# Performance work log

Measured on AMD Instinct MI355X. Metric: run time of the kernel, lower is better.

## Reference

```python
import jax, jax.numpy as jnp
import numpy as np

DIM = 256
HID = 128


def setup_inputs() -> dict:
    key = jax.random.key(0)
    ks = jax.random.split(key, 10)
    B, T = 8, 2048
    s_in = 1.0 / np.sqrt(DIM)
    s_h = 1.0 / np.sqrt(HID)
    return {
        "x": jax.random.normal(ks[0], (B, T, DIM), jnp.float32),
        "adapt_bias": jax.random.normal(ks[1], (B, T, T), jnp.float32),
        "Wq": jax.random.uniform(ks[2], (HID, DIM), jnp.float32, -s_in, s_in),
        "bq": jax.random.uniform(ks[3], (HID,), jnp.float32, -s_in, s_in),
        "Wk": jax.random.uniform(ks[4], (HID, DIM), jnp.float32, -s_in, s_in),
        "bk": jax.random.uniform(ks[5], (HID,), jnp.float32, -s_in, s_in),
        "Wv": jax.random.uniform(ks[6], (HID, DIM), jnp.float32, -s_in, s_in),
        "bv": jax.random.uniform(ks[7], (HID,), jnp.float32, -s_in, s_in),
        "Wp": jax.random.uniform(ks[8], (DIM, HID), jnp.float32, -s_h, s_h),
        "bp": jax.random.uniform(ks[9], (DIM,), jnp.float32, -s_h, s_h),
    }


def reference(x, adapt_bias, Wq, bq, Wk, bk, Wv, bv, Wp, bp):
    # y = x (default). Q,K,V: [B,T,H]
    Q = jnp.einsum('btd,hd->bth', x, Wq) + bq
    K = jnp.einsum('btd,hd->bth', x, Wk) + bk
    V = jnp.einsum('btd,hd->bth', x, Wv) + bv
    Q_sig = jax.nn.sigmoid(Q)
    ab = jax.nn.softmax(adapt_bias, axis=-1)        # [B,T,T]
    Ksm = jax.nn.softmax(K, axis=1)                 # softmax over time dim
    eab = jnp.exp(ab)                               # [B,T,T]
    eK = jnp.exp(Ksm)                               # [B,T,H]
    num = jnp.einsum('bts,bsh->bth', eab, eK * V)
    den = jnp.einsum('bts,bsh->bth', eab, eK)
    Yt = Q_sig * (num / den)                        # [B,T,H]
    return jnp.einsum('bth,dh->btd', Yt, Wp) + bp   # [B,T,DIM]
```

## Files before the change

### kernel.cpp

```cpp
#include <hip/hip_runtime.h>
#include <hip/hip_bf16.h>

#define B_ 8
#define T_ 2048
#define D_ 256
#define H_ 128

typedef float f32x4 __attribute__((ext_vector_type(4)));
typedef short bf16x8 __attribute__((ext_vector_type(8)));

__device__ __forceinline__ unsigned short f2bf(float f){
  union { float f; unsigned u; } v; v.f = f;
  unsigned u = v.u;
  unsigned r = (u + 0x7FFFu + ((u >> 16) & 1u)) >> 16;
  return (unsigned short)r;
}

#define GLL16(g, l) __builtin_amdgcn_global_load_lds( \
    (const __attribute__((address_space(1))) void*)(g), \
    (__attribute__((address_space(3))) void*)(l), 16, 0, 0)

__device__ __forceinline__ float blk_reduce(float v, bool is_max, float* sbuf){
  for(int o = 32; o > 0; o >>= 1){
    float t = __shfl_xor(v, o);
    v = is_max ? fmaxf(v, t) : (v + t);
  }
  int w = threadIdx.x >> 6;
  __syncthreads();
  if((threadIdx.x & 63) == 0) sbuf[w] = v;
  __syncthreads();
  float r = sbuf[0];
  for(int i = 1; i < 4; i++) r = is_max ? fmaxf(r, sbuf[i]) : (r + sbuf[i]);
  return r;
}

__global__ __launch_bounds__(256) void qkv_kernel(
    const float* __restrict__ x,
    const float* __restrict__ Wq, const float* __restrict__ bq,
    const float* __restrict__ Wk, const float* __restrict__ bk,
    const float* __restrict__ Wv, const float* __restrict__ bv,
    float* __restrict__ Qsig, float* __restrict__ Kt, float* __restrict__ Vt)
{
  const int mat = blockIdx.y;
  const int g0  = blockIdx.x * 64;
  const int tid = threadIdx.x;
  const float* W   = (mat == 0) ? Wq : (mat == 1) ? Wk : Wv;
  const float* bia = (mat == 0) ? bq : (mat == 1) ? bk : bv;

  __shared__ __align__(16) short As[64 * 32];
  __shared__ __align__(16) short Ws[128 * 32];
  __shared__ float tbuf[64][129];

  const int w = tid >> 6, lane = tid & 63, rl = lane & 15, kg = lane >> 4;
  f32x4 acc[8];
  for(int i = 0; i < 8; i++) acc[i] = (f32x4){0.f, 0.f, 0.f, 0.f};

  const int c = tid & 31, r8 = tid >> 5;
  for(int kk = 0; kk < 256; kk += 32){
    __syncthreads();
    for(int p = 0; p < 8; p++){
      int rr = r8 + p * 8;
      As[rr * 32 + c] = (short)f2bf(x[(size_t)(g0 + rr) * 256 + kk + c]);
    }
    for(int p = 0; p < 16; p++){
      int hh = r8 + p * 8;
      Ws[hh * 32 + c] = (short)f2bf(W[(size_t)hh * 256 + kk + c]);
    }
    __syncthreads();
    bf16x8 a = *(const bf16x8*)&As[(w * 16 + rl) * 32 + kg * 8];
    for(int cf = 0; cf < 8; cf++){
      bf16x8 bb = *(const bf16x8*)&Ws[(cf * 16 + rl) * 32 + kg * 8];
      acc[cf] = __builtin_amdgcn_mfma_f32_16x16x32_bf16(a, bb, acc[cf], 0, 0, 0);
    }
  }

  const int b = g0 >> 11, t0 = g0 & 2047;
  if(mat == 0){
    for(int cf = 0; cf < 8; cf++){
      int h = cf * 16 + rl;
      float bh = bia[h];
      for(int r = 0; r < 4; r++){
        int tl = w * 16 + kg * 4 + r;
        float v = acc[cf][r] + bh;
        Qsig[(size_t)(g0 + tl) * 128 + h] = 1.f / (1.f + __expf(-v));
      }
    }
  } else {
    for(int cf = 0; cf < 8; cf++){
      int h = cf * 16 + rl;
      float bh = bia[h];
      for(int r = 0; r < 4; r++){
        int tl = w * 16 + kg * 4 + r;
        tbuf[tl][h] = acc[cf][r] + bh;
      }
    }
    __syncthreads();
    float* dst = (mat == 1) ? Kt : Vt;
    int h = tid >> 1, part = tid & 1;
    float* drow = dst + (size_t)(b * 128 + h) * 2048 + t0 + part * 32;
    for(int i = 0; i < 32; i += 4){
      float4 o;
      o.x = tbuf[part * 32 + i + 0][h];
      o.y = tbuf[part * 32 + i + 1][h];
      o.z = tbuf[part * 32 + i + 2][h];
      o.w = tbuf[part * 32 + i + 3][h];
      *(float4*)(drow + i) = o;
    }
  }
}

__global__ __launch_bounds__(256) void colsm_kernel(
    const float* __restrict__ Kt, const float* __restrict__ Vt,
    unsigned short* __restrict__ Mt)
{
  __shared__ float sbuf[4];
  const int b  = blockIdx.x >> 5;
  const int hg = blockIdx.x & 31;
  const int tid = threadIdx.x;
  for(int i = 0; i < 4; i++){
    int h = hg * 4 + i;
    const float* kr = Kt + (size_t)(b * 128 + h) * 2048;
    const float* vr = Vt + (size_t)(b * 128 + h) * 2048;
    float4 k0 = *(const float4*)(kr + tid * 4);
    float4 k1 = *(const float4*)(kr + tid * 4 + 1024);
    float m = fmaxf(fmaxf(fmaxf(k0.x, k0.y), fmaxf(k0.z, k0.w)),
                    fmaxf(fmaxf(k1.x, k1.y), fmaxf(k1.z, k1.w)));
    m = blk_reduce(m, true, sbuf);
    float s = __expf(k0.x - m) + __expf(k0.y - m) + __expf(k0.z - m) + __expf(k0.w - m)
            + __expf(k1.x - m) + __expf(k1.y - m) + __expf(k1.z - m) + __expf(k1.w - m);
    s = blk_reduce(s, false, sbuf);
    float iz = 1.f / s;
    float4 v0 = *(const float4*)(vr + tid * 4);
    float4 v1 = *(const float4*)(vr + tid * 4 + 1024);
    unsigned short* ekvp = Mt + (size_t)(b * 256 + h) * 2048;
    unsigned short* ekp  = Mt + (size_t)(b * 256 + 128 + h) * 2048;
    ushort4 pv, pe;
    float e;
    e = __expf(__expf(k0.x - m) * iz); pv.x = f2bf(e * v0.x); pe.x = f2bf(e);
    e = __expf(__expf(k0.y - m) * iz); pv.y = f2bf(e * v0.y); pe.y = f2bf(e);
    e = __expf(__expf(k0.z - m) * iz); pv.z = f2bf(e * v0.z); pe.z = f2bf(e);
    e = __expf(__expf(k0.w - m) * iz); pv.w = f2bf(e * v0.w); pe.w = f2bf(e);
    ((ushort4*)ekvp)[tid] = pv;
    ((ushort4*)ekp)[tid]  = pe;
    e = __expf(__expf(k1.x - m) * iz); pv.x = f2bf(e * v1.x); pe.x = f2bf(e);
    e = __expf(__expf(k1.y - m) * iz); pv.y = f2bf(e * v1.y); pe.y = f2bf(e);
    e = __expf(__expf(k1.z - m) * iz); pv.z = f2bf(e * v1.z); pe.z = f2bf(e);
    e = __expf(__expf(k1.w - m) * iz); pv.w = f2bf(e * v1.w); pe.w = f2bf(e);
    ((ushort4*)ekvp)[tid + 256] = pv;
    ((ushort4*)ekp)[tid + 256]  = pe;
  }
}

__global__ __launch_bounds__(256) void softexp_kernel(
    const float* __restrict__ ab, unsigned short* __restrict__ eab)
{
  __shared__ float sbuf[4];
  const size_t row = blockIdx.x;
  const float* r = ab + row * 2048;
  const int tid = threadIdx.x;
  float4 v0 = *(const float4*)(r + tid * 4);
  float4 v1 = *(const float4*)(r + tid * 4 + 1024);
  float m = fmaxf(fmaxf(fmaxf(v0.x, v0.y), fmaxf(v0.z, v0.w)),
                  fmaxf(fmaxf(v1.x, v1.y), fmaxf(v1.z, v1.w)));
  m = blk_reduce(m, true, sbuf);
  float e0x = __expf(v0.x - m), e0y = __expf(v0.y - m);
  float e0z = __expf(v0.z - m), e0w = __expf(v0.w - m);
  float e1x = __expf(v1.x - m), e1y = __expf(v1.y - m);
  float e1z = __expf(v1.z - m), e1w = __expf(v1.w - m);
  float s = e0x + e0y + e0z + e0w + e1x + e1y + e1z + e1w;
  s = blk_reduce(s, false, sbuf);
  float iz = 1.f / s;
  ushort4 o;
  o.x = f2bf(__expf(e0x * iz)); o.y = f2bf(__expf(e0y * iz));
  o.z = f2bf(__expf(e0z * iz)); o.w = f2bf(__expf(e0w * iz));
  *(ushort4*)(eab + row * 2048 + tid * 4) = o;
  o.x = f2bf(__expf(e1x * iz)); o.y = f2bf(__expf(e1y * iz));
  o.z = f2bf(__expf(e1z * iz)); o.w = f2bf(__expf(e1w * iz));
  *(ushort4*)(eab + row * 2048 + tid * 4 + 1024) = o;
}

__global__ __launch_bounds__(256) void aft_gemm3(
    const unsigned short* __restrict__ eab,
    const unsigned short* __restrict__ Mt,
    const float* __restrict__ Qsig,
    unsigned short* __restrict__ Yt)
{
  __shared__ __align__(16) unsigned short As2[2][64 * 64];
  __shared__ __align__(16) unsigned short Bs2[2][128 * 64];

  const int bid = blockIdx.x;
  const int b   = bid & 7;
  const int idx = bid >> 3;
  const int rt  = idx >> 1;
  const int hb  = idx & 1;
  const int t0  = rt * 64;
  const int h0  = hb * 64;

  const int tid = threadIdx.x;
  const int w = tid >> 6, lane = tid & 63;
  const int rl = lane & 15, kg = lane >> 4;
  const int wr = w >> 1, wc = w & 1;

  const int lr = lane >> 3;
  const int cc = (lane & 7) ^ lr;

  const size_t rowbase = (size_t)b * 2048 + t0;
  const unsigned short* a_src = eab + (rowbase + (size_t)(w * 16 + lr)) * 2048 + cc * 8;
  const int mtrow = (w < 2) ? (h0 + w * 32 + lr) : (128 + h0 + (w - 2) * 32 + lr);
  const unsigned short* b_src = Mt + ((size_t)b * 256 + mtrow) * 2048 + cc * 8;

  f32x4 acc[2][4];
#pragma unroll
  for(int i = 0; i < 2; i++)
#pragma unroll
    for(int j = 0; j < 4; j++) acc[i][j] = (f32x4){0.f, 0.f, 0.f, 0.f};

  auto stage = [&](int buf, int t){
#pragma unroll
    for(int i = 0; i < 2; i++)
      GLL16(a_src + (size_t)i * 8 * 2048 + t * 64, &As2[buf][(w * 16 + i * 8) * 64]);
#pragma unroll
    for(int i = 0; i < 4; i++)
      GLL16(b_src + (size_t)i * 8 * 2048 + t * 64, &Bs2[buf][(w * 32 + i * 8) * 64]);
  };

  const int rx = rl & 7;
  stage(0, 0);
  __syncthreads();

  for(int t = 0; t < 32; ++t){
    const int cur = t & 1;
    if(t < 31) stage(cur ^ 1, t + 1);
#pragma unroll
    for(int ks = 0; ks < 2; ++ks){
      const int slot = ((ks * 4 + kg) ^ rx) * 8;
      bf16x8 a0 = *(const bf16x8*)&As2[cur][(wr * 32 + rl) * 64 + slot];
      bf16x8 a1 = *(const bf16x8*)&As2[cur][(wr * 32 + 16 + rl) * 64 + slot];
#pragma unroll
      for(int cf = 0; cf < 4; ++cf){
        const int brow = ((cf < 2) ? (wc * 32 + cf * 16)
                                   : (64 + wc * 32 + (cf - 2) * 16)) + rl;
        bf16x8 bb = *(const bf16x8*)&Bs2[cur][brow * 64 + slot];
        acc[0][cf] = __builtin_amdgcn_mfma_f32_16x16x32_bf16(a0, bb, acc[0][cf], 0, 0, 0);
        acc[1][cf] = __builtin_amdgcn_mfma_f32_16x16x32_bf16(a1, bb, acc[1][cf], 0, 0, 0);
      }
    }
    __syncthreads();
  }

#pragma unroll
  for(int rf = 0; rf < 2; ++rf)
#pragma unroll
    for(int cf = 0; cf < 2; ++cf){
      const int h = h0 + wc * 32 + cf * 16 + rl;
#pragma unroll
      for(int r = 0; r < 4; ++r){
        const int tl = wr * 32 + rf * 16 + kg * 4 + r;
        const size_t g = rowbase + tl;
        float num = acc[rf][cf][r], den = acc[rf][cf + 2][r];
        float q = Qsig[g * 128 + h];
        Yt[g * 128 + h] = f2bf(q * num / den);
      }
    }
}

__global__ __launch_bounds__(256) void outproj_kernel(
    const unsigned short* __restrict__ Yt, const float* __restrict__ Wp,
    const float* __restrict__ bp, float* __restrict__ out)
{
  __shared__ __align__(16) short As[64 * 32];
  __shared__ __align__(16) short Bs[256 * 32];
  const int g0 = blockIdx.x * 64;
  const int tid = threadIdx.x;
  const int w = tid >> 6, lane = tid & 63, rl = lane & 15, kg = lane >> 4;
  f32x4 acc[16];
  for(int i = 0; i < 16; i++) acc[i] = (f32x4){0.f, 0.f, 0.f, 0.f};

  const int ar = tid >> 2, apart = tid & 3;
  const int c = tid & 31, dr = tid >> 5;
  for(int k = 0; k < 128; k += 32){
    __syncthreads();
    *(uint4*)&As[ar * 32 + apart * 8] =
        *(const uint4*)(Yt + (size_t)(g0 + ar) * 128 + k + apart * 8);
    for(int p = 0; p < 32; p++){
      int d = dr + p * 8;
      Bs[d * 32 + c] = (short)f2bf(Wp[(size_t)d * 128 + k + c]);
    }
    __syncthreads();
    bf16x8 a = *(const bf16x8*)&As[(w * 16 + rl) * 32 + kg * 8];
    for(int cf = 0; cf < 16; cf++){
      bf16x8 bb = *(const bf16x8*)&Bs[(cf * 16 + rl) * 32 + kg * 8];
      acc[cf] = __builtin_amdgcn_mfma_f32_16x16x32_bf16(a, bb, acc[cf], 0, 0, 0);
    }
  }
  for(int cf = 0; cf < 16; cf++){
    int d = cf * 16 + rl;
    float bpd = bp[d];
    for(int r = 0; r < 4; r++){
      int tl = w * 16 + kg * 4 + r;
      out[(size_t)(g0 + tl) * 256 + d] = acc[cf][r] + bpd;
    }
  }
}

extern "C" void kernel_launch(void* const* d_in, const int* in_sizes, int n_in,
                              void* d_out, int out_size, void* d_ws, size_t ws_size,
                              hipStream_t stream)
{
  const float* x  = (const float*)d_in[0];
  const float* ab = (const float*)d_in[1];
  const float* Wq = (const float*)d_in[2];
  const float* bq = (const float*)d_in[3];
  const float* Wk = (const float*)d_in[4];
  const float* bk = (const float*)d_in[5];
  const float* Wv = (const float*)d_in[6];
  const float* bv = (const float*)d_in[7];
  const float* Wp = (const float*)d_in[8];
  const float* bp = (const float*)d_in[9];
  float* out = (float*)d_out;

  char* ws = (char*)d_ws;
  float* Qsig          = (float*)(ws);
  float* Kt            = (float*)(ws + 8388608);
  float* Vt            = (float*)(ws + 16777216);
  unsigned short* Mt   = (unsigned short*)(ws + 25165824);
  unsigned short* eab  = (unsigned short*)(ws + 33554432);
  unsigned short* Yt   = (unsigned short*)(ws + 8388608);

  qkv_kernel<<<dim3(256, 3), 256, 0, stream>>>(x, Wq, bq, Wk, bk, Wv, bv, Qsig, Kt, Vt);
  colsm_kernel<<<256, 256, 0, stream>>>(Kt, Vt, Mt);
  softexp_kernel<<<16384, 256, 0, stream>>>(ab, eab);
  aft_gemm3<<<512, 256, 0, stream>>>(eab, Mt, Qsig, Yt);
  outproj_kernel<<<256, 256, 0, stream>>>(Yt, Wp, bp, out);
}
```

Before: 103.2 us.

## Prefetch two tiles ahead in AFT GEMM with explicit waitcnt and split barriers

Restructures the AFT GEMM main loop so global-to-LDS loads are issued two K-tiles ahead instead of one. Explicit vmcnt waits replace full syncthreads. Fragments are read from LDS into registers before a barrier, so the freed buffer can be refilled while MFMAs run at raised wave priority. This targets exposed global memory latency in the memory-bound GEMM, at the cost of more register pressure and reliance on hand-counted vmcnt values.

```diff
diff --git a/kernel.cpp b/kernel.cpp
--- a/kernel.cpp
+++ b/kernel.cpp
@@ -179,7 +179,7 @@
   *(ushort4*)(eab + row * 2048 + tid * 4 + 1024) = o;
 }
 
-__global__ __launch_bounds__(256) void aft_gemm3(
+__global__ __launch_bounds__(256) void aft_gemm4(
     const unsigned short* __restrict__ eab,
     const unsigned short* __restrict__ Mt,
     const float* __restrict__ Qsig,
@@ -226,26 +226,44 @@
 
   const int rx = rl & 7;
   stage(0, 0);
-  __syncthreads();
+  stage(1, 1);
 
   for(int t = 0; t < 32; ++t){
     const int cur = t & 1;
-    if(t < 31) stage(cur ^ 1, t + 1);
+    if(t < 31) asm volatile("s_waitcnt vmcnt(6)" ::: "memory");
+    else       asm volatile("s_waitcnt vmcnt(0)" ::: "memory");
+    __builtin_amdgcn_s_barrier();
+    asm volatile("" ::: "memory");
+
+    bf16x8 af[2][2], bf[2][4];
 #pragma unroll
     for(int ks = 0; ks < 2; ++ks){
       const int slot = ((ks * 4 + kg) ^ rx) * 8;
-      bf16x8 a0 = *(const bf16x8*)&As2[cur][(wr * 32 + rl) * 64 + slot];
-      bf16x8 a1 = *(const bf16x8*)&As2[cur][(wr * 32 + 16 + rl) * 64 + slot];
+      af[ks][0] = *(const bf16x8*)&As2[cur][(wr * 32 + rl) * 64 + slot];
+      af[ks][1] = *(const bf16x8*)&As2[cur][(wr * 32 + 16 + rl) * 64 + slot];
 #pragma unroll
       for(int cf = 0; cf < 4; ++cf){
         const int brow = ((cf < 2) ? (wc * 32 + cf * 16)
                                    : (64 + wc * 32 + (cf - 2) * 16)) + rl;
-        bf16x8 bb = *(const bf16x8*)&Bs2[cur][brow * 64 + slot];
-        acc[0][cf] = __builtin_amdgcn_mfma_f32_16x16x32_bf16(a0, bb, acc[0][cf], 0, 0, 0);
-        acc[1][cf] = __builtin_amdgcn_mfma_f32_16x16x32_bf16(a1, bb, acc[1][cf], 0, 0, 0);
-      }
-    }
-    __syncthreads();
+        bf[ks][cf] = *(const bf16x8*)&Bs2[cur][brow * 64 + slot];
+      }
+    }
+    asm volatile("s_waitcnt lgkmcnt(0)" ::: "memory");
+    __builtin_amdgcn_sched_barrier(0);
+    __builtin_amdgcn_s_barrier();
+    asm volatile("" ::: "memory");
+
+    if(t < 30) stage(cur, t + 2);
+
+    __builtin_amdgcn_s_setprio(1);
+#pragma unroll
+    for(int ks = 0; ks < 2; ++ks)
+#pragma unroll
+      for(int cf = 0; cf < 4; ++cf){
+        acc[0][cf] = __builtin_amdgcn_mfma_f32_16x16x32_bf16(af[ks][0], bf[ks][cf], acc[0][cf], 0, 0, 0);
+        acc[1][cf] = __builtin_amdgcn_mfma_f32_16x16x32_bf16(af[ks][1], bf[ks][cf], acc[1][cf], 0, 0, 0);
+      }
+    __builtin_amdgcn_s_setprio(0);
   }
 
 #pragma unroll
@@ -330,6 +348,6 @@
   qkv_kernel<<<dim3(256, 3), 256, 0, stream>>>(x, Wq, bq, Wk, bk, Wv, bv, Qsig, Kt, Vt);
   colsm_kernel<<<256, 256, 0, stream>>>(Kt, Vt, Mt);
   softexp_kernel<<<16384, 256, 0, stream>>>(ab, eab);
-  aft_gemm3<<<512, 256, 0, stream>>>(eab, Mt, Qsig, Yt);
+  aft_gemm4<<<512, 256, 0, stream>>>(eab, Mt, Qsig, Yt);
   outproj_kernel<<<256, 256, 0, stream>>>(Yt, Wp, bp, out);
 }
```

New measurement: 96.51 us. 1.07x faster.

## Triple-buffer AFT GEMM with vmcnt waits and store K/V intermediates as bf16

Applied to the files above, without the earlier changes.

The main GEMM moves from a double-buffered LDS pipeline with two full syncthreads per iteration to a three-stage ring. It prefetches two tiles ahead, waits with explicit vmcnt counts plus a single barrier, and raises wave priority around the MFMA section, aiming to hide global-to-LDS load latency. Separately, the K and V intermediates are written and read as bf16 instead of fp32, halving traffic between the projection and column-softmax kernels. The cost is more LDS use and a reduction in K precision before the softmax and exp, which can shift numerical accuracy.

```diff
diff --git a/kernel.cpp b/kernel.cpp
--- a/kernel.cpp
+++ b/kernel.cpp
@@ -8,12 +8,17 @@
 
 typedef float f32x4 __attribute__((ext_vector_type(4)));
 typedef short bf16x8 __attribute__((ext_vector_type(8)));
+typedef unsigned short u16x8 __attribute__((ext_vector_type(8)));
 
 __device__ __forceinline__ unsigned short f2bf(float f){
   union { float f; unsigned u; } v; v.f = f;
   unsigned u = v.u;
   unsigned r = (u + 0x7FFFu + ((u >> 16) & 1u)) >> 16;
   return (unsigned short)r;
+}
+
+__device__ __forceinline__ float bf2f(unsigned short us){
+  union { unsigned u; float f; } v; v.u = ((unsigned)us) << 16; return v.f;
 }
 
 #define GLL16(g, l) __builtin_amdgcn_global_load_lds( \
@@ -39,7 +44,8 @@
     const float* __restrict__ Wq, const float* __restrict__ bq,
     const float* __restrict__ Wk, const float* __restrict__ bk,
     const float* __restrict__ Wv, const float* __restrict__ bv,
-    float* __restrict__ Qsig, float* __restrict__ Kt, float* __restrict__ Vt)
+    float* __restrict__ Qsig, unsigned short* __restrict__ Ktb,
+    unsigned short* __restrict__ Vtb)
 {
   const int mat = blockIdx.y;
   const int g0  = blockIdx.x * 64;
@@ -95,22 +101,21 @@
       }
     }
     __syncthreads();
-    float* dst = (mat == 1) ? Kt : Vt;
+    unsigned short* dst = (mat == 1) ? Ktb : Vtb;
     int h = tid >> 1, part = tid & 1;
-    float* drow = dst + (size_t)(b * 128 + h) * 2048 + t0 + part * 32;
-    for(int i = 0; i < 32; i += 4){
-      float4 o;
-      o.x = tbuf[part * 32 + i + 0][h];
-      o.y = tbuf[part * 32 + i + 1][h];
-      o.z = tbuf[part * 32 + i + 2][h];
-      o.w = tbuf[part * 32 + i + 3][h];
-      *(float4*)(drow + i) = o;
+    unsigned short* drow = dst + (size_t)(b * 128 + h) * 2048 + t0 + part * 32;
+#pragma unroll
+    for(int i = 0; i < 32; i += 8){
+      u16x8 o;
+#pragma unroll
+      for(int j = 0; j < 8; j++) o[j] = f2bf(tbuf[part * 32 + i + j][h]);
+      *(u16x8*)(drow + i) = o;
     }
   }
 }
 
 __global__ __launch_bounds__(256) void colsm_kernel(
-    const float* __restrict__ Kt, const float* __restrict__ Vt,
+    const unsigned short* __restrict__ Ktb, const unsigned short* __restrict__ Vtb,
     unsigned short* __restrict__ Mt)
 {
   __shared__ float sbuf[4];
@@ -119,35 +124,31 @@
   const int tid = threadIdx.x;
   for(int i = 0; i < 4; i++){
     int h = hg * 4 + i;
-    const float* kr = Kt + (size_t)(b * 128 + h) * 2048;
-    const float* vr = Vt + (size_t)(b * 128 + h) * 2048;
-    float4 k0 = *(const float4*)(kr + tid * 4);
-    float4 k1 = *(const float4*)(kr + tid * 4 + 1024);
-    float m = fmaxf(fmaxf(fmaxf(k0.x, k0.y), fmaxf(k0.z, k0.w)),
-                    fmaxf(fmaxf(k1.x, k1.y), fmaxf(k1.z, k1.w)));
+    const unsigned short* kr = Ktb + (size_t)(b * 128 + h) * 2048;
+    const unsigned short* vr = Vtb + (size_t)(b * 128 + h) * 2048;
+    u16x8 k8 = *(const u16x8*)(kr + tid * 8);
+    u16x8 v8 = *(const u16x8*)(vr + tid * 8);
+    float kf[8];
+#pragma unroll
+    for(int j = 0; j < 8; j++) kf[j] = bf2f(k8[j]);
+    float m = kf[0];
+#pragma unroll
+    for(int j = 1; j < 8; j++) m = fmaxf(m, kf[j]);
     m = blk_reduce(m, true, sbuf);
-    float s = __expf(k0.x - m) + __expf(k0.y - m) + __expf(k0.z - m) + __expf(k0.w - m)
-            + __expf(k1.x - m) + __expf(k1.y - m) + __expf(k1.z - m) + __expf(k1.w - m);
+    float s = 0.f;
+#pragma unroll
+    for(int j = 0; j < 8; j++) s += __expf(kf[j] - m);
     s = blk_reduce(s, false, sbuf);
     float iz = 1.f / s;
-    float4 v0 = *(const float4*)(vr + tid * 4);
-    float4 v1 = *(const float4*)(vr + tid * 4 + 1024);
-    unsigned short* ekvp = Mt + (size_t)(b * 256 + h) * 2048;
-    unsigned short* ekp  = Mt + (size_t)(b * 256 + 128 + h) * 2048;
-    ushort4 pv, pe;
-    float e;
-    e = __expf(__expf(k0.x - m) * iz); pv.x = f2bf(e * v0.x); pe.x = f2bf(e);
-    e = __expf(__expf(k0.y - m) * iz); pv.y = f2bf(e * v0.y); pe.y = f2bf(e);
-    e = __expf(__expf(k0.z - m) * iz); pv.z = f2bf(e * v0.z); pe.z = f2bf(e);
-    e = __expf(__expf(k0.w - m) * iz); pv.w = f2bf(e * v0.w); pe.w = f2bf(e);
-    ((ushort4*)ekvp)[tid] = pv;
-    ((ushort4*)ekp)[tid]  = pe;
-    e = __expf(__expf(k1.x - m) * iz); pv.x = f2bf(e * v1.x); pe.x = f2bf(e);
-    e = __expf(__expf(k1.y - m) * iz); pv.y = f2bf(e * v1.y); pe.y = f2bf(e);
-    e = __expf(__expf(k1.z - m) * iz); pv.z = f2bf(e * v1.z); pe.z = f2bf(e);
-    e = __expf(__expf(k1.w - m) * iz); pv.w = f2bf(e * v1.w); pe.w = f2bf(e);
-    ((ushort4*)ekvp)[tid + 256] = pv;
-    ((ushort4*)ekp)[tid + 256]  = pe;
+    u16x8 pv, pe;
+#pragma unroll
+    for(int j = 0; j < 8; j++){
+      float e = __expf(__expf(kf[j] - m) * iz);
+      pv[j] = f2bf(e * bf2f(v8[j]));
+      pe[j] = f2bf(e);
+    }
+    *(u16x8*)(Mt + (size_t)(b * 256 + h) * 2048 + tid * 8) = pv;
+    *(u16x8*)(Mt + (size_t)(b * 256 + 128 + h) * 2048 + tid * 8) = pe;
   }
 }
 
@@ -179,14 +180,14 @@
   *(ushort4*)(eab + row * 2048 + tid * 4 + 1024) = o;
 }
 
-__global__ __launch_bounds__(256) void aft_gemm3(
+__global__ __launch_bounds__(256) void aft_gemm6(
     const unsigned short* __restrict__ eab,
     const unsigned short* __restrict__ Mt,
     const float* __restrict__ Qsig,
     unsigned short* __restrict__ Yt)
 {
-  __shared__ __align__(16) unsigned short As2[2][64 * 64];
-  __shared__ __align__(16) unsigned short Bs2[2][128 * 64];
+  __shared__ __align__(16) unsigned short As2[3][64 * 64];
+  __shared__ __align__(16) unsigned short Bs2[3][128 * 64];
 
   const int bid = blockIdx.x;
   const int b   = bid & 7;
@@ -226,11 +227,18 @@
 
   const int rx = rl & 7;
   stage(0, 0);
-  __syncthreads();
-
+  stage(1, 1);
+
+  int cur = 0;
   for(int t = 0; t < 32; ++t){
-    const int cur = t & 1;
-    if(t < 31) stage(cur ^ 1, t + 1);
+    if(t < 31) asm volatile("s_waitcnt vmcnt(6)" ::: "memory");
+    else       asm volatile("s_waitcnt vmcnt(0)" ::: "memory");
+    __builtin_amdgcn_s_barrier();
+    if(t < 30){
+      int nb = cur + 2; if(nb >= 3) nb -= 3;
+      stage(nb, t + 2);
+    }
+    __builtin_amdgcn_s_setprio(1);
 #pragma unroll
     for(int ks = 0; ks < 2; ++ks){
       const int slot = ((ks * 4 + kg) ^ rx) * 8;
@@ -245,7 +253,10 @@
         acc[1][cf] = __builtin_amdgcn_mfma_f32_16x16x32_bf16(a1, bb, acc[1][cf], 0, 0, 0);
       }
     }
-    __syncthreads();
+    __builtin_amdgcn_s_setprio(0);
+    asm volatile("s_waitcnt lgkmcnt(0)" ::: "memory");
+    __builtin_amdgcn_sched_barrier(0);
+    cur += 1; if(cur >= 3) cur -= 3;
   }
 
 #pragma unroll
@@ -321,15 +332,15 @@
 
   char* ws = (char*)d_ws;
   float* Qsig          = (float*)(ws);
-  float* Kt            = (float*)(ws + 8388608);
-  float* Vt            = (float*)(ws + 16777216);
-  unsigned short* Mt   = (unsigned short*)(ws + 25165824);
-  unsigned short* eab  = (unsigned short*)(ws + 33554432);
+  unsigned short* Ktb  = (unsigned short*)(ws + 8388608);
+  unsigned short* Vtb  = (unsigned short*)(ws + 12582912);
+  unsigned short* Mt   = (unsigned short*)(ws + 16777216);
+  unsigned short* eab  = (unsigned short*)(ws + 25165824);
   unsigned short* Yt   = (unsigned short*)(ws + 8388608);
 
-  qkv_kernel<<<dim3(256, 3), 256, 0, stream>>>(x, Wq, bq, Wk, bk, Wv, bv, Qsig, Kt, Vt);
-  colsm_kernel<<<256, 256, 0, stream>>>(Kt, Vt, Mt);
+  qkv_kernel<<<dim3(256, 3), 256, 0, stream>>>(x, Wq, bq, Wk, bk, Wv, bv, Qsig, Ktb, Vtb);
+  colsm_kernel<<<256, 256, 0, stream>>>(Ktb, Vtb, Mt);
   softexp_kernel<<<16384, 256, 0, stream>>>(ab, eab);
-  aft_gemm3<<<512, 256, 0, stream>>>(eab, Mt, Qsig, Yt);
+  aft_gemm6<<<512, 256, 0, stream>>>(eab, Mt, Qsig, Yt);
   outproj_kernel<<<256, 256, 0, stream>>>(Yt, Wp, bp, out);
 }
```

After: 97.45 us. 1.06x faster.
